# Optimization experiments

Measured on AMD Instinct MI355X. Metric: run time of the kernel, lower is better.

Reference implementation:

```python
import jax, jax.numpy as jnp
import numpy as np

N_NODES = 20000
N_EDGES = 320000
IN_FEATS = 64
HIDDENS = [128, 128, 128]
K = 4        # n_kernels
DIM = 2      # pseudo_coord


def setup_inputs() -> dict:
    key = jax.random.key(0)
    ks = jax.random.split(key, 32)
    inp = {
        "features": jax.random.normal(ks[0], (N_NODES, IN_FEATS), dtype=jnp.float32),
        "pseudo": jax.random.uniform(ks[1], (N_EDGES, DIM), dtype=jnp.float32),
        "src": jax.random.randint(ks[2], (N_EDGES,), 0, N_NODES, dtype=jnp.int32),
        "dst": jax.random.randint(ks[3], (N_EDGES,), 0, N_NODES, dtype=jnp.int32),
    }
    dims_in = [IN_FEATS] + HIDDENS[:-1]
    ki = 4
    for i, (din, dout) in enumerate(zip(dims_in, HIDDENS)):
        inp[f"fc_w{i}"] = jax.random.normal(ks[ki], (din, K * dout), dtype=jnp.float32) * (1.0 / np.sqrt(din)); ki += 1
        inp[f"mu{i}"] = jax.random.normal(ks[ki], (K, DIM), dtype=jnp.float32) * 0.1; ki += 1
        inp[f"inv_sigma{i}"] = jnp.ones((K, DIM), dtype=jnp.float32)
        inp[f"bias{i}"] = jnp.zeros((dout,), dtype=jnp.float32)
        inp[f"pw{i}"] = jax.random.normal(ks[ki], (DIM, DIM), dtype=jnp.float32) * 0.5; ki += 1
        inp[f"pb{i}"] = jnp.zeros((DIM,), dtype=jnp.float32)
    return inp


def _gmm_layer(h, pseudo, src, dst, fc_w, mu, inv_sigma, bias, pw, pb):
    k, dim = mu.shape
    dout = fc_w.shape[1] // k
    hp = (h @ fc_w).reshape(-1, k, dout)              # [N, K, out]
    u = jnp.tanh(pseudo @ pw + pb)                    # [E, dim] per-layer pseudo projection
    diff = (u[:, None, :] - mu[None, :, :]) * inv_sigma[None, :, :]
    w = jnp.exp(-0.5 * jnp.sum(diff * diff, axis=-1))  # [E, K] Gaussian mixture weights
    msg = jnp.einsum('ek,eko->eo', w, hp[src])         # gather + weighted mix -> [E, out]
    agg = jax.ops.segment_sum(msg, dst, num_segments=h.shape[0])  # scatter-sum
    return agg + bias


def reference(features, pseudo, src, dst,
              fc_w0, mu0, inv_sigma0, bias0, pw0, pb0,
              fc_w1, mu1, inv_sigma1, bias1, pw1, pb1,
              fc_w2, mu2, inv_sigma2, bias2, pw2, pb2):
    h = features
    h = _gmm_layer(h, pseudo, src, dst, fc_w0, mu0, inv_sigma0, bias0, pw0, pb0)
    h = _gmm_layer(h, pseudo, src, dst, fc_w1, mu1, inv_sigma1, bias1, pw1, pb1)
    h = _gmm_layer(h, pseudo, src, dst, fc_w2, mu2, inv_sigma2, bias2, pw2, pb2)
    return h
```

## Files before the change

### kernel.cpp

```cpp
#include <hip/hip_runtime.h>
#include <hip/hip_bf16.h>
#include <hip/hip_fp16.h>
#include <math.h>

#define NN 20000
#define NE 320000
#define SLOT 64

typedef __attribute__((ext_vector_type(8))) short bf16x8;
typedef __attribute__((ext_vector_type(4))) float f32x4;

__device__ inline float bf2f_lo(uint v) {
    union { uint i; float f; } c; c.i = v << 16; return c.f;
}
__device__ inline float bf2f_hi(uint v) {
    union { uint i; float f; } c; c.i = v & 0xffff0000u; return c.f;
}
__device__ inline ushort f2bf(float f) {
    __hip_bfloat16 h = __float2bfloat16(f);
    return *reinterpret_cast<ushort*>(&h);
}
__device__ inline float2 h2f2(uint u) {
    union { uint i; __half2 h; } c; c.i = u;
    return __half22float2(c.h);
}
__device__ inline ushort f2h(float f) {
    __half h = __float2half_rn(f);
    return *reinterpret_cast<ushort*>(&h);
}

__device__ inline float fast_tanh(float x) {
    x = fminf(fmaxf(x, -9.f), 9.f);
    float e = __expf(2.f * x);
    return 1.f - 2.f / (e + 1.f);
}

struct EdgeParams {
    const float *pw0, *pb0, *mu0, *is0;
    const float *pw1, *pb1, *mu1, *is1;
    const float *pw2, *pb2, *mu2, *is2;
};

__device__ inline void layer_w(float p0, float p1, const float* pw, const float* pb,
                               const float* mu, const float* is, float* out4) {
    float u0 = fast_tanh(p0 * pw[0] + p1 * pw[2] + pb[0]);
    float u1 = fast_tanh(p0 * pw[1] + p1 * pw[3] + pb[1]);
#pragma unroll
    for (int k = 0; k < 4; ++k) {
        float d0 = (u0 - mu[k * 2 + 0]) * is[k * 2 + 0];
        float d1 = (u1 - mu[k * 2 + 1]) * is[k * 2 + 1];
        out4[k] = __expf(-0.5f * (d0 * d0 + d1 * d1));
    }
}

__global__ void fill_prep(const int* __restrict__ dst, const int* __restrict__ src,
                          const float* __restrict__ pseudo, EdgeParams P,
                          int* __restrict__ cursor, int* __restrict__ csr_src,
                          ushort* __restrict__ cw0, ushort* __restrict__ cw1,
                          ushort* __restrict__ cw2,
                          const float* __restrict__ f0, const float* __restrict__ f1,
                          const float* __restrict__ f2, ushort* __restrict__ w0,
                          ushort* __restrict__ w1, ushort* __restrict__ w2) {
    int bid = blockIdx.x;
    if (bid < 1250) {
        int e = bid * 256 + threadIdx.x;
        int n = dst[e];
        int pos = atomicAdd(&cursor[n], 1);
        if (pos < SLOT) {
            int slot = n * SLOT + pos;
            csr_src[slot] = src[e];
            float2 p = *(const float2*)(pseudo + (size_t)e * 2);
            float w[4];
            uint2 pk;
            layer_w(p.x, p.y, P.pw0, P.pb0, P.mu0, P.is0, w);
            pk.x = (uint)f2h(w[0]) | ((uint)f2h(w[1]) << 16);
            pk.y = (uint)f2h(w[2]) | ((uint)f2h(w[3]) << 16);
            *(uint2*)(cw0 + (size_t)slot * 4) = pk;
            layer_w(p.x, p.y, P.pw1, P.pb1, P.mu1, P.is1, w);
            pk.x = (uint)f2h(w[0]) | ((uint)f2h(w[1]) << 16);
            pk.y = (uint)f2h(w[2]) | ((uint)f2h(w[3]) << 16);
            *(uint2*)(cw1 + (size_t)slot * 4) = pk;
            layer_w(p.x, p.y, P.pw2, P.pb2, P.mu2, P.is2, w);
            pk.x = (uint)f2h(w[0]) | ((uint)f2h(w[1]) << 16);
            pk.y = (uint)f2h(w[2]) | ((uint)f2h(w[3]) << 16);
            *(uint2*)(cw2 + (size_t)slot * 4) = pk;
        }
    } else {
        int idx = (bid - 1250) * 256 + threadIdx.x;
        const float* srcp;
        ushort* dstp;
        int din, KD, li;
        if (idx < 128 * 256) {
            srcp = f0; dstp = w0; din = 64; KD = 256; li = idx;
        } else if (idx < 128 * 256 + 128 * 512) {
            srcp = f1; dstp = w1; din = 128; KD = 512; li = idx - 128 * 256;
        } else {
            srcp = f2; dstp = w2; din = 128; KD = 512; li = idx - 128 * 256 - 128 * 512;
        }
        int n = li / KD;
        int r = li - n * KD;
        int k = r / din;
        int d = r - k * din;
        dstp[li] = f2bf(srcp[d * 512 + k * 128 + n]);
    }
}

template <int DIN, bool INF32, bool OUTBF>
__global__ __launch_bounds__(1024, 4) void layer_fused(
    const void* __restrict__ hin, const int* __restrict__ cursor,
    const int* __restrict__ csr_src, const ushort* __restrict__ csr_w,
    const ushort* __restrict__ Bt, const float* __restrict__ bias,
    void* __restrict__ hout) {
    constexpr int KD = 4 * DIN;
    constexpr int PITCH = KD + 8;
    constexpr int B = 8;
    __shared__ __align__(16) ushort Ts[16 * PITCH];
    int wv = threadIdx.x >> 6, lane = threadIdx.x & 63;
    int l16 = lane & 15, quad = lane >> 4;
    int nb = blockIdx.x * 16;
    int n = nb + wv;

    int deg = __builtin_amdgcn_readfirstlane(cursor[n]);
    deg = deg < SLOT ? deg : SLOT;
    int base = n * SLOT;

    if (INF32) {
        const float* h = (const float*)hin;
        float a0 = 0.f, a1 = 0.f, a2 = 0.f, a3 = 0.f;
        for (int i = 0; i < deg; i += B) {
            int s[B]; uint wlo[B], whi[B]; float hv[B];
#pragma unroll
            for (int u = 0; u < B; ++u) {
                bool ok = (i + u) < deg;
                int idx = base + (ok ? i + u : 0);
                s[u] = csr_src[idx];
                uint2 wp = *(const uint2*)(csr_w + (size_t)idx * 4);
                wlo[u] = ok ? wp.x : 0u;
                whi[u] = ok ? wp.y : 0u;
            }
#pragma unroll
            for (int u = 0; u < B; ++u) hv[u] = h[(size_t)s[u] * 64 + lane];
#pragma unroll
            for (int u = 0; u < B; ++u) {
                float2 wa = h2f2(wlo[u]);
                float2 wb = h2f2(whi[u]);
                a0 += wa.x * hv[u];
                a1 += wa.y * hv[u];
                a2 += wb.x * hv[u];
                a3 += wb.y * hv[u];
            }
        }
        Ts[wv * PITCH + 0 * 64 + lane] = f2bf(a0);
        Ts[wv * PITCH + 1 * 64 + lane] = f2bf(a1);
        Ts[wv * PITCH + 2 * 64 + lane] = f2bf(a2);
        Ts[wv * PITCH + 3 * 64 + lane] = f2bf(a3);
    } else {
        const ushort* h = (const ushort*)hin;
        float a00 = 0.f, a01 = 0.f, a10 = 0.f, a11 = 0.f;
        float a20 = 0.f, a21 = 0.f, a30 = 0.f, a31 = 0.f;
        for (int i = 0; i < deg; i += B) {
            int s[B]; uint wlo[B], whi[B]; uint v[B];
#pragma unroll
            for (int u = 0; u < B; ++u) {
                bool ok = (i + u) < deg;
                int idx = base + (ok ? i + u : 0);
                s[u] = csr_src[idx];
                uint2 wp = *(const uint2*)(csr_w + (size_t)idx * 4);
                wlo[u] = ok ? wp.x : 0u;
                whi[u] = ok ? wp.y : 0u;
            }
#pragma unroll
            for (int u = 0; u < B; ++u)
                v[u] = *(const uint*)(h + (size_t)s[u] * DIN + lane * 2);
#pragma unroll
            for (int u = 0; u < B; ++u) {
                float2 wa = h2f2(wlo[u]);
                float2 wb = h2f2(whi[u]);
                float lo = bf2f_lo(v[u]), hi = bf2f_hi(v[u]);
                a00 += wa.x * lo; a01 += wa.x * hi;
                a10 += wa.y * lo; a11 += wa.y * hi;
                a20 += wb.x * lo; a21 += wb.x * hi;
                a30 += wb.y * lo; a31 += wb.y * hi;
            }
        }
        ushort2 p;
        p.x = f2bf(a00); p.y = f2bf(a01);
        *(ushort2*)(Ts + wv * PITCH + 0 * DIN + lane * 2) = p;
        p.x = f2bf(a10); p.y = f2bf(a11);
        *(ushort2*)(Ts + wv * PITCH + 1 * DIN + lane * 2) = p;
        p.x = f2bf(a20); p.y = f2bf(a21);
        *(ushort2*)(Ts + wv * PITCH + 2 * DIN + lane * 2) = p;
        p.x = f2bf(a30); p.y = f2bf(a31);
        *(ushort2*)(Ts + wv * PITCH + 3 * DIN + lane * 2) = p;
    }
    __syncthreads();

    if (wv < 8) {
        int c0 = wv * 16;
        f32x4 acc = (f32x4){0.f, 0.f, 0.f, 0.f};
#pragma unroll 4
        for (int k0 = 0; k0 < KD; k0 += 32) {
            bf16x8 af = *(const bf16x8*)(Ts + l16 * PITCH + k0 + quad * 8);
            bf16x8 bfr = *(const bf16x8*)(Bt + (size_t)(c0 + l16) * KD + k0 + quad * 8);
            acc = __builtin_amdgcn_mfma_f32_16x16x32_bf16(af, bfr, acc, 0, 0, 0);
        }
        int gn = c0 + l16;
        float bv = bias[gn];
#pragma unroll
        for (int i = 0; i < 4; ++i) {
            int gm = nb + quad * 4 + i;
            float val = acc[i] + bv;
            if (OUTBF)
                ((ushort*)hout)[(size_t)gm * 128 + gn] = f2bf(val);
            else
                ((float*)hout)[(size_t)gm * 128 + gn] = val;
        }
    }
}

extern "C" void kernel_launch(void* const* d_in, const int* in_sizes, int n_in,
                              void* d_out, int out_size, void* d_ws, size_t ws_size,
                              hipStream_t stream) {
    const float* features = (const float*)d_in[0];
    const float* pseudo = (const float*)d_in[1];
    const int* src = (const int*)d_in[2];
    const int* dst = (const int*)d_in[3];
    const float* fc_w[3] = {(const float*)d_in[4], (const float*)d_in[10], (const float*)d_in[16]};
    const float* mu[3] = {(const float*)d_in[5], (const float*)d_in[11], (const float*)d_in[17]};
    const float* isg[3] = {(const float*)d_in[6], (const float*)d_in[12], (const float*)d_in[18]};
    const float* bias[3] = {(const float*)d_in[7], (const float*)d_in[13], (const float*)d_in[19]};
    const float* pw[3] = {(const float*)d_in[8], (const float*)d_in[14], (const float*)d_in[20]};
    const float* pb[3] = {(const float*)d_in[9], (const float*)d_in[15], (const float*)d_in[21]};

    char* ws = (char*)d_ws;
    auto alloc = [&](size_t bytes) -> void* {
        void* p = (void*)ws;
        ws += (bytes + 255) & ~(size_t)255;
        return p;
    };
    int* cursor = (int*)alloc((size_t)NN * 4);
    int* csr_src = (int*)alloc((size_t)NN * SLOT * 4);
    ushort* cw0 = (ushort*)alloc((size_t)NN * SLOT * 8);
    ushort* cw1 = (ushort*)alloc((size_t)NN * SLOT * 8);
    ushort* cw2 = (ushort*)alloc((size_t)NN * SLOT * 8);
    ushort* w2t_0 = (ushort*)alloc((size_t)128 * 256 * 2);
    ushort* w2t_1 = (ushort*)alloc((size_t)128 * 512 * 2);
    ushort* w2t_2 = (ushort*)alloc((size_t)128 * 512 * 2);
    ushort* h1 = (ushort*)alloc((size_t)NN * 128 * 2);
    ushort* h2 = (ushort*)alloc((size_t)NN * 128 * 2);

    hipMemsetAsync(cursor, 0, (size_t)NN * 4, stream);
    EdgeParams P;
    P.pw0 = pw[0]; P.pb0 = pb[0]; P.mu0 = mu[0]; P.is0 = isg[0];
    P.pw1 = pw[1]; P.pb1 = pb[1]; P.mu1 = mu[1]; P.is1 = isg[1];
    P.pw2 = pw[2]; P.pb2 = pb[2]; P.mu2 = mu[2]; P.is2 = isg[2];
    fill_prep<<<1890, 256, 0, stream>>>(dst, src, pseudo, P, cursor, csr_src,
                                        cw0, cw1, cw2,
                                        fc_w[0], fc_w[1], fc_w[2], w2t_0, w2t_1, w2t_2);

    const int GB = NN / 16;

    layer_fused<64, true, true><<<GB, 1024, 0, stream>>>(
        features, cursor, csr_src, cw0, w2t_0, bias[0], h1);
    layer_fused<128, false, true><<<GB, 1024, 0, stream>>>(
        h1, cursor, csr_src, cw1, w2t_1, bias[1], h2);
    layer_fused<128, false, false><<<GB, 1024, 0, stream>>>(
        h2, cursor, csr_src, cw2, w2t_2, bias[2], (float*)d_out);
}
```

Before: 244.3 us.

## Interleave edge records, convert features to bf16, split wave into two edge halves

Packs each edge's source index and the three layers' fp16 mixture weights into one 32-byte record, replacing separate src and weight arrays. The input features are converted to bf16 in the prep kernel so layer 0 gathers half as many bytes. In the gather loop each half-wave handles alternating edges with wider per-lane loads, and the two halves are combined with a cross-lane shuffle. This is meant to cut gather bytes and raise memory-level parallelism, but each layer now also reads the padding and the other layers' weights in every record. It also adds an extra bf16 rounding of the layer-0 input.

```diff
diff --git a/kernel.cpp b/kernel.cpp
--- a/kernel.cpp
+++ b/kernel.cpp
@@ -19,6 +19,9 @@
 __device__ inline ushort f2bf(float f) {
     __hip_bfloat16 h = __float2bfloat16(f);
     return *reinterpret_cast<ushort*>(&h);
+}
+__device__ inline uint pack2bf(float a, float b) {
+    return (uint)f2bf(a) | ((uint)f2bf(b) << 16);
 }
 __device__ inline float2 h2f2(uint u) {
     union { uint i; __half2 h; } c; c.i = u;
@@ -55,9 +58,8 @@
 
 __global__ void fill_prep(const int* __restrict__ dst, const int* __restrict__ src,
                           const float* __restrict__ pseudo, EdgeParams P,
-                          int* __restrict__ cursor, int* __restrict__ csr_src,
-                          ushort* __restrict__ cw0, ushort* __restrict__ cw1,
-                          ushort* __restrict__ cw2,
+                          int* __restrict__ cursor, uint* __restrict__ recs,
+                          const float* __restrict__ features, ushort* __restrict__ fbf,
                           const float* __restrict__ f0, const float* __restrict__ f1,
                           const float* __restrict__ f2, ushort* __restrict__ w0,
                           ushort* __restrict__ w1, ushort* __restrict__ w2) {
@@ -67,25 +69,24 @@
         int n = dst[e];
         int pos = atomicAdd(&cursor[n], 1);
         if (pos < SLOT) {
-            int slot = n * SLOT + pos;
-            csr_src[slot] = src[e];
+            size_t slot = (size_t)n * SLOT + pos;
             float2 p = *(const float2*)(pseudo + (size_t)e * 2);
             float w[4];
-            uint2 pk;
+            uint pk0x, pk0y, pk1x, pk1y, pk2x, pk2y;
             layer_w(p.x, p.y, P.pw0, P.pb0, P.mu0, P.is0, w);
-            pk.x = (uint)f2h(w[0]) | ((uint)f2h(w[1]) << 16);
-            pk.y = (uint)f2h(w[2]) | ((uint)f2h(w[3]) << 16);
-            *(uint2*)(cw0 + (size_t)slot * 4) = pk;
+            pk0x = (uint)f2h(w[0]) | ((uint)f2h(w[1]) << 16);
+            pk0y = (uint)f2h(w[2]) | ((uint)f2h(w[3]) << 16);
             layer_w(p.x, p.y, P.pw1, P.pb1, P.mu1, P.is1, w);
-            pk.x = (uint)f2h(w[0]) | ((uint)f2h(w[1]) << 16);
-            pk.y = (uint)f2h(w[2]) | ((uint)f2h(w[3]) << 16);
-            *(uint2*)(cw1 + (size_t)slot * 4) = pk;
+            pk1x = (uint)f2h(w[0]) | ((uint)f2h(w[1]) << 16);
+            pk1y = (uint)f2h(w[2]) | ((uint)f2h(w[3]) << 16);
             layer_w(p.x, p.y, P.pw2, P.pb2, P.mu2, P.is2, w);
-            pk.x = (uint)f2h(w[0]) | ((uint)f2h(w[1]) << 16);
-            pk.y = (uint)f2h(w[2]) | ((uint)f2h(w[3]) << 16);
-            *(uint2*)(cw2 + (size_t)slot * 4) = pk;
-        }
-    } else {
+            pk2x = (uint)f2h(w[0]) | ((uint)f2h(w[1]) << 16);
+            pk2y = (uint)f2h(w[2]) | ((uint)f2h(w[3]) << 16);
+            uint* r = recs + slot * 8;
+            *(uint4*)(r + 0) = make_uint4((uint)src[e], 0u, pk0x, pk0y);
+            *(uint4*)(r + 4) = make_uint4(pk1x, pk1y, pk2x, pk2y);
+        }
+    } else if (bid < 1890) {
         int idx = (bid - 1250) * 256 + threadIdx.x;
         const float* srcp;
         ushort* dstp;
@@ -102,114 +103,130 @@
         int k = r / din;
         int d = r - k * din;
         dstp[li] = f2bf(srcp[d * 512 + k * 128 + n]);
-    }
-}
-
-template <int DIN, bool INF32, bool OUTBF>
+    } else {
+        int idx = (bid - 1890) * 256 + threadIdx.x;
+        size_t b8 = (size_t)idx * 8;
+        float4 a = *(const float4*)(features + b8);
+        float4 b = *(const float4*)(features + b8 + 4);
+        uint4 o;
+        o.x = pack2bf(a.x, a.y);
+        o.y = pack2bf(a.z, a.w);
+        o.z = pack2bf(b.x, b.y);
+        o.w = pack2bf(b.z, b.w);
+        *(uint4*)(fbf + b8) = o;
+    }
+}
+
+template <int DIN, bool OUTBF>
 __global__ __launch_bounds__(1024, 4) void layer_fused(
-    const void* __restrict__ hin, const int* __restrict__ cursor,
-    const int* __restrict__ csr_src, const ushort* __restrict__ csr_w,
+    const ushort* __restrict__ hbf, const int* __restrict__ cursor,
+    const uint* __restrict__ recs, int woff,
     const ushort* __restrict__ Bt, const float* __restrict__ bias,
     void* __restrict__ hout) {
     constexpr int KD = 4 * DIN;
     constexpr int PITCH = KD + 8;
     constexpr int B = 8;
+    constexpr int FPL = DIN / 32;
     __shared__ __align__(16) ushort Ts[16 * PITCH];
     int wv = threadIdx.x >> 6, lane = threadIdx.x & 63;
     int l16 = lane & 15, quad = lane >> 4;
+    int half = lane >> 5, l32 = lane & 31;
     int nb = blockIdx.x * 16;
     int n = nb + wv;
 
     int deg = __builtin_amdgcn_readfirstlane(cursor[n]);
     deg = deg < SLOT ? deg : SLOT;
-    int base = n * SLOT;
-
-    if (INF32) {
-        const float* h = (const float*)hin;
-        float a0 = 0.f, a1 = 0.f, a2 = 0.f, a3 = 0.f;
-        for (int i = 0; i < deg; i += B) {
-            int s[B]; uint wlo[B], whi[B]; float hv[B];
-#pragma unroll
-            for (int u = 0; u < B; ++u) {
-                bool ok = (i + u) < deg;
-                int idx = base + (ok ? i + u : 0);
-                s[u] = csr_src[idx];
-                uint2 wp = *(const uint2*)(csr_w + (size_t)idx * 4);
-                wlo[u] = ok ? wp.x : 0u;
-                whi[u] = ok ? wp.y : 0u;
+    size_t base = (size_t)n * SLOT;
+
+    float acc[4 * FPL];
+#pragma unroll
+    for (int j = 0; j < 4 * FPL; ++j) acc[j] = 0.f;
+
+    for (int i = 0; i < deg; i += 2 * B) {
+        int s[B];
+        uint wlo[B], whi[B];
+        uint2 hv[B];
+#pragma unroll
+        for (int u = 0; u < B; ++u) {
+            int ii = i + 2 * u + half;
+            bool ok = ii < deg;
+            size_t idx = base + (ok ? ii : 0);
+            const uint* r = recs + idx * 8;
+            s[u] = (int)r[0];
+            uint2 wp = *(const uint2*)(r + woff);
+            wlo[u] = ok ? wp.x : 0u;
+            whi[u] = ok ? wp.y : 0u;
+        }
+#pragma unroll
+        for (int u = 0; u < B; ++u) {
+            const ushort* row = hbf + (size_t)s[u] * DIN + l32 * FPL;
+            if (DIN == 64)
+                hv[u].x = *(const uint*)row;
+            else
+                hv[u] = *(const uint2*)row;
+        }
+#pragma unroll
+        for (int u = 0; u < B; ++u) {
+            float2 wa = h2f2(wlo[u]);
+            float2 wb = h2f2(whi[u]);
+            float w0 = wa.x, w1 = wa.y, w2 = wb.x, w3 = wb.y;
+            float fx0 = bf2f_lo(hv[u].x), fx1 = bf2f_hi(hv[u].x);
+            if (DIN == 64) {
+                acc[0] += w0 * fx0; acc[1] += w0 * fx1;
+                acc[2] += w1 * fx0; acc[3] += w1 * fx1;
+                acc[4] += w2 * fx0; acc[5] += w2 * fx1;
+                acc[6] += w3 * fx0; acc[7] += w3 * fx1;
+            } else {
+                float fx2 = bf2f_lo(hv[u].y), fx3 = bf2f_hi(hv[u].y);
+                acc[0] += w0 * fx0;  acc[1] += w0 * fx1;
+                acc[2] += w0 * fx2;  acc[3] += w0 * fx3;
+                acc[4] += w1 * fx0;  acc[5] += w1 * fx1;
+                acc[6] += w1 * fx2;  acc[7] += w1 * fx3;
+                acc[8] += w2 * fx0;  acc[9] += w2 * fx1;
+                acc[10] += w2 * fx2; acc[11] += w2 * fx3;
+                acc[12] += w3 * fx0; acc[13] += w3 * fx1;
+                acc[14] += w3 * fx2; acc[15] += w3 * fx3;
             }
-#pragma unroll
-            for (int u = 0; u < B; ++u) hv[u] = h[(size_t)s[u] * 64 + lane];
-#pragma unroll
-            for (int u = 0; u < B; ++u) {
-                float2 wa = h2f2(wlo[u]);
-                float2 wb = h2f2(whi[u]);
-                a0 += wa.x * hv[u];
-                a1 += wa.y * hv[u];
-                a2 += wb.x * hv[u];
-                a3 += wb.y * hv[u];
+        }
+    }
+#pragma unroll
+    for (int j = 0; j < 4 * FPL; ++j) acc[j] += __shfl_xor(acc[j], 32);
+
+    if (half == 0) {
+#pragma unroll
+        for (int k = 0; k < 4; ++k) {
+            if (DIN == 64) {
+                ushort2 p;
+                p.x = f2bf(acc[k * 2 + 0]);
+                p.y = f2bf(acc[k * 2 + 1]);
+                *(ushort2*)(Ts + wv * PITCH + k * DIN + l32 * 2) = p;
+            } else {
+                ushort4 p;
+                p.x = f2bf(acc[k * 4 + 0]);
+                p.y = f2bf(acc[k * 4 + 1]);
+                p.z = f2bf(acc[k * 4 + 2]);
+                p.w = f2bf(acc[k * 4 + 3]);
+                *(ushort4*)(Ts + wv * PITCH + k * DIN + l32 * 4) = p;
             }
         }
-        Ts[wv * PITCH + 0 * 64 + lane] = f2bf(a0);
-        Ts[wv * PITCH + 1 * 64 + lane] = f2bf(a1);
-        Ts[wv * PITCH + 2 * 64 + lane] = f2bf(a2);
-        Ts[wv * PITCH + 3 * 64 + lane] = f2bf(a3);
-    } else {
-        const ushort* h = (const ushort*)hin;
-        float a00 = 0.f, a01 = 0.f, a10 = 0.f, a11 = 0.f;
-        float a20 = 0.f, a21 = 0.f, a30 = 0.f, a31 = 0.f;
-        for (int i = 0; i < deg; i += B) {
-            int s[B]; uint wlo[B], whi[B]; uint v[B];
-#pragma unroll
-            for (int u = 0; u < B; ++u) {
-                bool ok = (i + u) < deg;
-                int idx = base + (ok ? i + u : 0);
-                s[u] = csr_src[idx];
-                uint2 wp = *(const uint2*)(csr_w + (size_t)idx * 4);
-                wlo[u] = ok ? wp.x : 0u;
-                whi[u] = ok ? wp.y : 0u;
-            }
-#pragma unroll
-            for (int u = 0; u < B; ++u)
-                v[u] = *(const uint*)(h + (size_t)s[u] * DIN + lane * 2);
-#pragma unroll
-            for (int u = 0; u < B; ++u) {
-                float2 wa = h2f2(wlo[u]);
-                float2 wb = h2f2(whi[u]);
-                float lo = bf2f_lo(v[u]), hi = bf2f_hi(v[u]);
-                a00 += wa.x * lo; a01 += wa.x * hi;
-                a10 += wa.y * lo; a11 += wa.y * hi;
-                a20 += wb.x * lo; a21 += wb.x * hi;
-                a30 += wb.y * lo; a31 += wb.y * hi;
-            }
-        }
-        ushort2 p;
-        p.x = f2bf(a00); p.y = f2bf(a01);
-        *(ushort2*)(Ts + wv * PITCH + 0 * DIN + lane * 2) = p;
-        p.x = f2bf(a10); p.y = f2bf(a11);
-        *(ushort2*)(Ts + wv * PITCH + 1 * DIN + lane * 2) = p;
-        p.x = f2bf(a20); p.y = f2bf(a21);
-        *(ushort2*)(Ts + wv * PITCH + 2 * DIN + lane * 2) = p;
-        p.x = f2bf(a30); p.y = f2bf(a31);
-        *(ushort2*)(Ts + wv * PITCH + 3 * DIN + lane * 2) = p;
     }
     __syncthreads();
 
     if (wv < 8) {
         int c0 = wv * 16;
-        f32x4 acc = (f32x4){0.f, 0.f, 0.f, 0.f};
+        f32x4 acc2 = (f32x4){0.f, 0.f, 0.f, 0.f};
 #pragma unroll 4
         for (int k0 = 0; k0 < KD; k0 += 32) {
             bf16x8 af = *(const bf16x8*)(Ts + l16 * PITCH + k0 + quad * 8);
             bf16x8 bfr = *(const bf16x8*)(Bt + (size_t)(c0 + l16) * KD + k0 + quad * 8);
-            acc = __builtin_amdgcn_mfma_f32_16x16x32_bf16(af, bfr, acc, 0, 0, 0);
+            acc2 = __builtin_amdgcn_mfma_f32_16x16x32_bf16(af, bfr, acc2, 0, 0, 0);
         }
         int gn = c0 + l16;
         float bv = bias[gn];
 #pragma unroll
         for (int i = 0; i < 4; ++i) {
             int gm = nb + quad * 4 + i;
-            float val = acc[i] + bv;
+            float val = acc2[i] + bv;
             if (OUTBF)
                 ((ushort*)hout)[(size_t)gm * 128 + gn] = f2bf(val);
             else
@@ -239,10 +256,8 @@
         return p;
     };
     int* cursor = (int*)alloc((size_t)NN * 4);
-    int* csr_src = (int*)alloc((size_t)NN * SLOT * 4);
-    ushort* cw0 = (ushort*)alloc((size_t)NN * SLOT * 8);
-    ushort* cw1 = (ushort*)alloc((size_t)NN * SLOT * 8);
-    ushort* cw2 = (ushort*)alloc((size_t)NN * SLOT * 8);
+    uint* recs = (uint*)alloc((size_t)NN * SLOT * 32);
+    ushort* fbf = (ushort*)alloc((size_t)NN * 64 * 2);
     ushort* w2t_0 = (ushort*)alloc((size_t)128 * 256 * 2);
     ushort* w2t_1 = (ushort*)alloc((size_t)128 * 512 * 2);
     ushort* w2t_2 = (ushort*)alloc((size_t)128 * 512 * 2);
@@ -254,16 +269,15 @@
     P.pw0 = pw[0]; P.pb0 = pb[0]; P.mu0 = mu[0]; P.is0 = isg[0];
     P.pw1 = pw[1]; P.pb1 = pb[1]; P.mu1 = mu[1]; P.is1 = isg[1];
     P.pw2 = pw[2]; P.pb2 = pb[2]; P.mu2 = mu[2]; P.is2 = isg[2];
-    fill_prep<<<1890, 256, 0, stream>>>(dst, src, pseudo, P, cursor, csr_src,
-                                        cw0, cw1, cw2,
+    fill_prep<<<2515, 256, 0, stream>>>(dst, src, pseudo, P, cursor, recs, features, fbf,
                                         fc_w[0], fc_w[1], fc_w[2], w2t_0, w2t_1, w2t_2);
 
     const int GB = NN / 16;
 
-    layer_fused<64, true, true><<<GB, 1024, 0, stream>>>(
-        features, cursor, csr_src, cw0, w2t_0, bias[0], h1);
-    layer_fused<128, false, true><<<GB, 1024, 0, stream>>>(
-        h1, cursor, csr_src, cw1, w2t_1, bias[1], h2);
-    layer_fused<128, false, false><<<GB, 1024, 0, stream>>>(
-        h2, cursor, csr_src, cw2, w2t_2, bias[2], (float*)d_out);
-}
+    layer_fused<64, true><<<GB, 1024, 0, stream>>>(
+        fbf, cursor, recs, 2, w2t_0, bias[0], h1);
+    layer_fused<128, true><<<GB, 1024, 0, stream>>>(
+        h1, cursor, recs, 4, w2t_1, bias[1], h2);
+    layer_fused<128, false><<<GB, 1024, 0, stream>>>(
+        h2, cursor, recs, 6, w2t_2, bias[2], (float*)d_out);
+}
```

Result: faster. 236.5 us (-3.2%).
